# Kernel tuning notes

Measured on AMD Instinct MI355X. Metric: run time of the kernel, lower is better.

## Reference

```python
import jax, jax.numpy as jnp
import numpy as np

PARAMETER = 0.1
INPUT_SIZE = 512
OUTPUT_SIZE = 512


def setup_inputs() -> dict:
    key = jax.random.key(0)
    k1, k2, k3 = jax.random.split(key, 3)
    T, B = 4096, 32
    input_tensor = jax.random.normal(k1, (T, B, INPUT_SIZE), dtype=jnp.float32)
    k = np.sqrt(1.0 / INPUT_SIZE)
    weight = jax.random.uniform(k2, (OUTPUT_SIZE, INPUT_SIZE), dtype=jnp.float32, minval=-k, maxval=k)
    bias = jax.random.uniform(k3, (OUTPUT_SIZE,), dtype=jnp.float32, minval=-k, maxval=k)
    return {"input_tensor": input_tensor, "weight": weight, "bias": bias}


def reference(input_tensor, weight, bias):
    # linear projection: [T, B, I] @ [I, O] -> [T, B, O]
    y = jnp.einsum('tbi,oi->tbo', input_tensor, weight) + bias

    # EMA recurrence: v[0] = y[0]; v[t] = p * v[t-1] + y[t]
    def step(carry, yt):
        v = PARAMETER * carry + yt
        return v, v

    _, rest = jax.lax.scan(step, y[0], y[1:])
    return jnp.concatenate([y[:1], rest], axis=0)
```

## Files before the change

### kernel.cpp

```cpp
#include <hip/hip_runtime.h>
#include <hip/hip_bf16.h>

#define T_DIM 4096
#define B_DIM 32
#define I_DIM 512
#define O_DIM 512
#define M_DIM (T_DIM * B_DIM)
#define PARAM 0.1f
#define ISCALE 1.1111112f

#define STRIP 32
#define TAPS 8

#define BM 256
#define BN 256
#define BK 64
#define NK (I_DIM / BK)

typedef __attribute__((ext_vector_type(8))) short bf16x8;
typedef __attribute__((ext_vector_type(4))) float f32x4;

__device__ __forceinline__ unsigned short f2bf(float f) {
    union { __hip_bfloat16 b; unsigned short u; } cv;
    cv.b = __float2bfloat16(f);
    return cv.u;
}

__global__ __launch_bounds__(256) void wcvt_kernel(const float* __restrict__ W,
                                                   unsigned short* __restrict__ Wb) {
    const int i = (blockIdx.x * 256 + threadIdx.x) * 4;
    f32x4 v = *(const f32x4*)(W + i);
    ushort4 o;
    o.x = f2bf(v[0]); o.y = f2bf(v[1]); o.z = f2bf(v[2]); o.w = f2bf(v[3]);
    *(ushort4*)(Wb + i) = o;
}

__global__ __launch_bounds__(256) void xema_kernel(const float* __restrict__ X,
                                                   unsigned short* __restrict__ Xv) {
    const int s   = blockIdx.x >> 4;
    const int blk = blockIdx.x & 15;
    const int col = (blk * 256 + threadIdx.x) * 4;
    const int t0  = s * STRIP;
    const int b   = col >> 9;
    const int o   = col & 511;

    const float* xin = X + (size_t)t0 * 16384 + col;
    unsigned short* xout = Xv + (size_t)(t0 * 32 + b) * 512 + o;

    f32x4 v = {0.f, 0.f, 0.f, 0.f};
    if (s > 0) {
        const float* w = xin - (size_t)TAPS * 16384;
        #pragma unroll
        for (int j = 0; j < TAPS; ++j)
            v = PARAM * v + *(const f32x4*)(w + (size_t)j * 16384);
    }

    f32x4 bufA[4], bufB[4];
    #pragma unroll
    for (int j = 0; j < 4; ++j) bufA[j] = *(const f32x4*)(xin + (size_t)j * 16384);

    #pragma unroll
    for (int i = 0; i < STRIP; i += 8) {
        #pragma unroll
        for (int j = 0; j < 4; ++j)
            bufB[j] = *(const f32x4*)(xin + (size_t)(i + 4 + j) * 16384);
        #pragma unroll
        for (int j = 0; j < 4; ++j) {
            v = PARAM * v + bufA[j];
            ushort4 pk; pk.x = f2bf(v[0]); pk.y = f2bf(v[1]); pk.z = f2bf(v[2]); pk.w = f2bf(v[3]);
            *(ushort4*)(xout + (size_t)(i + j) * 16384) = pk;
        }
        if (i + 8 < STRIP) {
            #pragma unroll
            for (int j = 0; j < 4; ++j)
                bufA[j] = *(const f32x4*)(xin + (size_t)(i + 8 + j) * 16384);
        }
        #pragma unroll
        for (int j = 0; j < 4; ++j) {
            v = PARAM * v + bufB[j];
            ushort4 pk; pk.x = f2bf(v[0]); pk.y = f2bf(v[1]); pk.z = f2bf(v[2]); pk.w = f2bf(v[3]);
            *(ushort4*)(xout + (size_t)(i + 4 + j) * 16384) = pk;
        }
    }
}

__global__ __launch_bounds__(512, 2) void gemm_kernel(const unsigned short* __restrict__ Xv,
                                                      const unsigned short* __restrict__ Wb,
                                                      const float* __restrict__ bias,
                                                      float* __restrict__ Y) {
    __shared__ __align__(16) short As[BM * BK];
    __shared__ __align__(16) short Bs[BN * BK];

    const int tid  = threadIdx.x;
    const int lane = tid & 63;
    const int wave = tid >> 6;
    const int wm   = wave >> 2;
    const int wn   = wave & 3;

    const int bid  = blockIdx.x;
    const int swz  = (bid & 7) * 128 + (bid >> 3);
    const int bn   = swz & 1;
    const int mt   = swz >> 1;
    const int row0 = mt * BM;
    const int col0 = bn * BN;

    const int cs = (tid & 7) ^ ((tid >> 3) & 7);
    const unsigned short* aSrc = Xv + (size_t)(row0 + (tid >> 3)) * 512 + cs * 8;
    const unsigned short* bSrc = Wb + (size_t)(col0 + (tid >> 3)) * 512 + cs * 8;

    f32x4 acc[8][4] = {};

    for (int ks = 0; ks < NK; ++ks) {
        const int k0 = ks * BK;
        #pragma unroll
        for (int s_ = 0; s_ < 4; ++s_)
            __builtin_amdgcn_global_load_lds(
                (const __attribute__((address_space(1))) unsigned int*)(aSrc + (size_t)s_ * 64 * 512 + k0),
                (__attribute__((address_space(3))) unsigned int*)(As + (s_ * 512 + tid) * 8),
                16, 0, 0);
        #pragma unroll
        for (int s_ = 0; s_ < 4; ++s_)
            __builtin_amdgcn_global_load_lds(
                (const __attribute__((address_space(1))) unsigned int*)(bSrc + (size_t)s_ * 64 * 512 + k0),
                (__attribute__((address_space(3))) unsigned int*)(Bs + (s_ * 512 + tid) * 8),
                16, 0, 0);
        __syncthreads();

        #pragma unroll
        for (int kk = 0; kk < 2; ++kk) {
            const int cc = kk * 4 + (lane >> 4);
            bf16x8 a_[8], b_[4];
            #pragma unroll
            for (int mf = 0; mf < 8; ++mf) {
                const int r = wm * 128 + mf * 16 + (lane & 15);
                a_[mf] = *(const bf16x8*)((const char*)As + r * 128 + ((cc ^ (r & 7)) << 4));
            }
            #pragma unroll
            for (int nf = 0; nf < 4; ++nf) {
                const int r = wn * 64 + nf * 16 + (lane & 15);
                b_[nf] = *(const bf16x8*)((const char*)Bs + r * 128 + ((cc ^ (r & 7)) << 4));
            }
            #pragma unroll
            for (int mf = 0; mf < 8; ++mf)
                #pragma unroll
                for (int nf = 0; nf < 4; ++nf)
                    acc[mf][nf] = __builtin_amdgcn_mfma_f32_16x16x32_bf16(
                        b_[nf], a_[mf], acc[mf][nf], 0, 0, 0);
        }
        __syncthreads();
    }

    float sc4[4];
    #pragma unroll
    for (int tt = 0; tt < 4; ++tt) {
        const int t_ = ((row0 + wm * 128) >> 5) + tt;
        sc4[tt] = (1.0f - __expf(-2.3025851f * (float)(t_ + 1))) * ISCALE;
    }
    f32x4 bvv[4];
    #pragma unroll
    for (int nf = 0; nf < 4; ++nf)
        bvv[nf] = *(const f32x4*)(bias + col0 + wn * 64 + nf * 16 + ((lane >> 4) << 2));

    #pragma unroll
    for (int mf = 0; mf < 8; ++mf) {
        const int grow = row0 + wm * 128 + mf * 16 + (lane & 15);
        const float sc = sc4[mf >> 1];
        #pragma unroll
        for (int nf = 0; nf < 4; ++nf) {
            const int gcol = col0 + wn * 64 + nf * 16 + ((lane >> 4) << 2);
            f32x4 out;
            #pragma unroll
            for (int e = 0; e < 4; ++e) out[e] = acc[mf][nf][e] + sc * bvv[nf][e];
            *(f32x4*)(Y + (size_t)grow * O_DIM + gcol) = out;
        }
    }
}

extern "C" void kernel_launch(void* const* d_in, const int* in_sizes, int n_in,
                              void* d_out, int out_size, void* d_ws, size_t ws_size,
                              hipStream_t stream) {
    const float* X    = (const float*)d_in[0];
    const float* W    = (const float*)d_in[1];
    const float* bias = (const float*)d_in[2];
    float* Y = (float*)d_out;
    unsigned short* Wb = (unsigned short*)d_ws;
    unsigned short* Xv = (unsigned short*)((char*)d_ws + (1 << 20));

    wcvt_kernel<<<dim3(O_DIM * I_DIM / (256 * 4)), dim3(256), 0, stream>>>(W, Wb);
    xema_kernel<<<dim3((T_DIM / STRIP) * 16), dim3(256), 0, stream>>>(X, Xv);
    gemm_kernel<<<dim3((M_DIM / BM) * (O_DIM / BN)), dim3(512), 0, stream>>>(Xv, Wb, bias, Y);
}
```

Measured before the change: 251.2 us.

## Double-buffer GEMM LDS tiles to prefetch the next K-slice during MFMA

The GEMM kernel now keeps two LDS buffers for the A and B tiles. It issues the global-to-LDS loads for the next K step before running the MFMAs on the current buffer, so the barrier that used to follow each load is gone. The goal is to hide global load latency behind the matrix math. The catch is that LDS use per block doubles to about 128 KB, so the two blocks per CU requested by the launch bounds can no longer both fit. That cuts occupancy and removes the overlap that previously came from running two blocks side by side.

```diff
diff --git a/kernel.cpp b/kernel.cpp
--- a/kernel.cpp
+++ b/kernel.cpp
@@ -88,8 +88,8 @@
                                                       const unsigned short* __restrict__ Wb,
                                                       const float* __restrict__ bias,
                                                       float* __restrict__ Y) {
-    __shared__ __align__(16) short As[BM * BK];
-    __shared__ __align__(16) short Bs[BN * BK];
+    __shared__ __align__(16) short As[2][BM * BK];
+    __shared__ __align__(16) short Bs[2][BN * BK];
 
     const int tid  = threadIdx.x;
     const int lane = tid & 63;
@@ -108,23 +108,31 @@
     const unsigned short* aSrc = Xv + (size_t)(row0 + (tid >> 3)) * 512 + cs * 8;
     const unsigned short* bSrc = Wb + (size_t)(col0 + (tid >> 3)) * 512 + cs * 8;
 
+    #define STAGE(d, kt)                                                              \
+        do {                                                                          \
+            _Pragma("unroll")                                                         \
+            for (int s_ = 0; s_ < 4; ++s_)                                            \
+                __builtin_amdgcn_global_load_lds(                                     \
+                    (const __attribute__((address_space(1))) unsigned int*)(aSrc + (size_t)s_ * 64 * 512 + (kt) * 64), \
+                    (__attribute__((address_space(3))) unsigned int*)(&As[d][0] + (s_ * 512 + tid) * 8),              \
+                    16, 0, 0);                                                        \
+            _Pragma("unroll")                                                         \
+            for (int s_ = 0; s_ < 4; ++s_)                                            \
+                __builtin_amdgcn_global_load_lds(                                     \
+                    (const __attribute__((address_space(1))) unsigned int*)(bSrc + (size_t)s_ * 64 * 512 + (kt) * 64), \
+                    (__attribute__((address_space(3))) unsigned int*)(&Bs[d][0] + (s_ * 512 + tid) * 8),              \
+                    16, 0, 0);                                                        \
+        } while (0)
+
     f32x4 acc[8][4] = {};
 
+    STAGE(0, 0);
+    __syncthreads();
+
     for (int ks = 0; ks < NK; ++ks) {
-        const int k0 = ks * BK;
-        #pragma unroll
-        for (int s_ = 0; s_ < 4; ++s_)
-            __builtin_amdgcn_global_load_lds(
-                (const __attribute__((address_space(1))) unsigned int*)(aSrc + (size_t)s_ * 64 * 512 + k0),
-                (__attribute__((address_space(3))) unsigned int*)(As + (s_ * 512 + tid) * 8),
-                16, 0, 0);
-        #pragma unroll
-        for (int s_ = 0; s_ < 4; ++s_)
-            __builtin_amdgcn_global_load_lds(
-                (const __attribute__((address_space(1))) unsigned int*)(bSrc + (size_t)s_ * 64 * 512 + k0),
-                (__attribute__((address_space(3))) unsigned int*)(Bs + (s_ * 512 + tid) * 8),
-                16, 0, 0);
-        __syncthreads();
+        const int cur = ks & 1;
+        if (ks < NK - 1)
+            STAGE(cur ^ 1, ks + 1);
 
         #pragma unroll
         for (int kk = 0; kk < 2; ++kk) {
@@ -133,12 +141,12 @@
             #pragma unroll
             for (int mf = 0; mf < 8; ++mf) {
                 const int r = wm * 128 + mf * 16 + (lane & 15);
-                a_[mf] = *(const bf16x8*)((const char*)As + r * 128 + ((cc ^ (r & 7)) << 4));
+                a_[mf] = *(const bf16x8*)((const char*)&As[cur][0] + r * 128 + ((cc ^ (r & 7)) << 4));
             }
             #pragma unroll
             for (int nf = 0; nf < 4; ++nf) {
                 const int r = wn * 64 + nf * 16 + (lane & 15);
-                b_[nf] = *(const bf16x8*)((const char*)Bs + r * 128 + ((cc ^ (r & 7)) << 4));
+                b_[nf] = *(const bf16x8*)((const char*)&Bs[cur][0] + r * 128 + ((cc ^ (r & 7)) << 4));
             }
             #pragma unroll
             for (int mf = 0; mf < 8; ++mf)
```

New measurement: 235.9 us. 6.1% less time.
